# Performance work log

Measured on AMD Instinct MI355X. Metric: run time of the kernel, lower is better.

Reference implementation:

```python
import jax, jax.numpy as jnp
import numpy as np

EPS = 1e-5

def _ln(x, g, b):
    mu = jnp.mean(x, axis=-1, keepdims=True)
    var = jnp.mean((x - mu) ** 2, axis=-1, keepdims=True)
    return (x - mu) / jnp.sqrt(var + EPS) * g + b

def _silu(x):
    return x * jax.nn.sigmoid(x)

def setup_inputs() -> dict:
    key = jax.random.key(0)
    ks = jax.random.split(key, 32)
    B = 131072
    def rn(k, shape, scale=0.05):
        return jax.random.normal(k, shape, dtype=jnp.float32) * scale
    inp = {
        'x': jax.random.normal(ks[0], (B, 90), dtype=jnp.float32),
        'w_emb': rn(ks[1], (24, 10)),
        'pos_d': rn(ks[2], (9, 24), 0.02),
        'pos_c': rn(ks[3], (3, 64), 0.02),
        'tw1': rn(ks[4], (256, 72)), 'tb1': rn(ks[5], (256,)),
        'tw2': rn(ks[6], (256, 256)), 'tb2': rn(ks[7], (256,)),
        'tw3': rn(ks[8], (64, 256)), 'tb3': jnp.zeros((64,), jnp.float32),
        'ln1g': jnp.ones((64,), jnp.float32), 'ln1b': jnp.zeros((64,), jnp.float32),
        'inpw': rn(ks[9], (192, 64)), 'inpb': rn(ks[10], (192,)),
        'outw': rn(ks[11], (64, 64)), 'outb': rn(ks[12], (64,)),
        'ln2g': jnp.ones((64,), jnp.float32), 'ln2b': jnp.zeros((64,), jnp.float32),
        'ffw1': rn(ks[13], (128, 64)), 'ffb1': rn(ks[14], (128,)),
        'ffw2': rn(ks[15], (64, 128)), 'ffb2': rn(ks[16], (64,)),
        'hw1': rn(ks[17], (160, 192)), 'hb1': rn(ks[18], (160,)),
        'hw2': rn(ks[19], (64, 160)), 'hb2': rn(ks[20], (64,)),
        'hw3': rn(ks[21], (1, 64)), 'hb3': jnp.zeros((1,), jnp.float32),
    }
    return inp

def reference(x, w_emb, pos_d, pos_c, tw1, tb1, tw2, tb2, tw3, tb3,
              ln1g, ln1b, inpw, inpb, outw, outb, ln2g, ln2b,
              ffw1, ffb1, ffw2, ffb2, hw1, hb1, hw2, hb2, hw3, hb3):
    B = x.shape[0]
    H, D = 4, 16  # heads, head_dim (embed 64)
    digits = x.reshape(B, 9, 10) @ w_emb.T + pos_d          # [B,9,24]
    chunks = digits.reshape(B, 3, 72)                        # [B,3,72]
    h = _silu(chunks @ tw1.T + tb1)                          # [B,3,256]
    h = _silu(h @ tw2.T + tb2)                               # [B,3,256]
    chunks = h @ tw3.T + tb3                                 # [B,3,64]
    chunks = chunks + pos_c
    a = _ln(chunks, ln1g, ln1b)
    qkv = a @ inpw.T + inpb                                  # [B,3,192]
    q, k, v = jnp.split(qkv, 3, axis=-1)
    q = q.reshape(B, 3, H, D).transpose(0, 2, 1, 3)
    k = k.reshape(B, 3, H, D).transpose(0, 2, 1, 3)
    v = v.reshape(B, 3, H, D).transpose(0, 2, 1, 3)
    scores = jnp.einsum('bhsd,bhtd->bhst', q, k) / jnp.sqrt(jnp.float32(D))
    attn = jax.nn.softmax(scores, axis=-1)
    o = jnp.einsum('bhst,bhtd->bhsd', attn, v)
    o = o.transpose(0, 2, 1, 3).reshape(B, 3, 64)
    attn_out = o @ outw.T + outb
    chunks = chunks + attn_out
    f = _ln(chunks, ln2g, ln2b)
    chunks = chunks + (_silu(f @ ffw1.T + ffb1) @ ffw2.T + ffb2)
    flat = chunks.reshape(B, 192)
    hh = _silu(flat @ hw1.T + hb1)
    hh = _silu(hh @ hw2.T + hb2)
    return hh @ hw3.T + hb3                                  # [B,1]
```

## Files before the change

### kernel.cpp

```cpp
#include <hip/hip_runtime.h>
#include <math.h>


typedef short s8v __attribute__((ext_vector_type(8)));
typedef float f4v __attribute__((ext_vector_type(4)));
typedef int   i2v __attribute__((ext_vector_type(2)));
typedef int   i4v __attribute__((ext_vector_type(4)));

__device__ __forceinline__ short f2bf(float f) {
    unsigned u = __float_as_uint(f);
    unsigned r = (u + 0x7fffu + ((u >> 16) & 1u)) >> 16;
    return (short)r;
}
__device__ __forceinline__ int cvt_pk_bf16(float a, float b) {
    int r;
    asm("v_cvt_pk_bf16_f32 %0, %1, %2" : "=v"(r) : "v"(a), "v"(b));
    return r;
}
__device__ __forceinline__ float silu_f(float v) {
    return v * __builtin_amdgcn_rcpf(1.0f + __expf(-v));
}

#define BARRIER() do {                                        \
    asm volatile("s_waitcnt lgkmcnt(0)" ::: "memory");        \
    __builtin_amdgcn_s_barrier();                             \
    __builtin_amdgcn_sched_barrier(0);                        \
} while (0)

#define OFF_T1F  0
#define OFF_TW2  8192
#define OFF_TW3  73728
#define OFF_INP  90112
#define OFF_OUT  102400
#define OFF_FF1  106496
#define OFF_FF2  114688
#define OFF_HW1  122880
#define OFF_HW2  153600
#define BIAS1_ELEM 163840

__global__ void pack_weights(const float* __restrict__ w_emb, const float* __restrict__ tw1,
                             const float* __restrict__ pos_d, const float* __restrict__ tb1,
                             const float* __restrict__ tw2, const float* __restrict__ tw3,
                             const float* __restrict__ inpw, const float* __restrict__ outw,
                             const float* __restrict__ ffw1, const float* __restrict__ ffw2,
                             const float* __restrict__ hw1, const float* __restrict__ hw2,
                             short* __restrict__ dst)
{
    int L = blockIdx.y;
    if (L == 0) {
        int total = 16 * 512;
        for (int e = blockIdx.x * blockDim.x + threadIdx.x; e < total; e += gridDim.x * blockDim.x) {
            int nt = e >> 9, q = e & 511;
            int l = q >> 3, j = q & 7;
            int n = nt * 16 + (l & 15);
            int k = (l >> 4) * 8 + j;
            float v = 0.f;
            if (k < 30) {
                int gl = k / 10, kk = k - gl * 10;
                const float* trow = tw1 + n * 72 + gl * 24;
                for (int jj = 0; jj < 24; ++jj) v += trow[jj] * w_emb[jj * 10 + kk];
            }
            dst[OFF_T1F + e] = f2bf(v);
        }
        return;
    }
    if (L == 9) {
        float* b1 = (float*)(dst + BIAS1_ELEM);
        for (int e = blockIdx.x * blockDim.x + threadIdx.x; e < 768; e += gridDim.x * blockDim.x) {
            int pos = e >> 8, n = e & 255;
            float v = tb1[n];
            for (int j = 0; j < 72; ++j)
                v += tw1[n * 72 + j] * pos_d[(pos * 3 + j / 24) * 24 + (j % 24)];
            b1[e] = v;
        }
        return;
    }
    const float* W; int K, KS, N, off;
    switch (L) {
      case 1: W = tw2;  K = 256; KS = 8; N = 256; off = OFF_TW2; break;
      case 2: W = tw3;  K = 256; KS = 8; N = 64;  off = OFF_TW3; break;
      case 3: W = inpw; K = 64;  KS = 2; N = 192; off = OFF_INP; break;
      case 4: W = outw; K = 64;  KS = 2; N = 64;  off = OFF_OUT; break;
      case 5: W = ffw1; K = 64;  KS = 2; N = 128; off = OFF_FF1; break;
      case 6: W = ffw2; K = 128; KS = 4; N = 64;  off = OFF_FF2; break;
      case 7: W = hw1;  K = 192; KS = 6; N = 160; off = OFF_HW1; break;
      default:W = hw2;  K = 160; KS = 5; N = 64;  off = OFF_HW2; break;
    }
    int total = (N >> 4) * KS * 512;
    for (int e = blockIdx.x * blockDim.x + threadIdx.x; e < total; e += gridDim.x * blockDim.x) {
        int nt = e / (KS * 512);
        int r  = e - nt * (KS * 512);
        int ks = r >> 9;
        int q  = r & 511;
        int l  = q >> 3, j = q & 7;
        int n  = nt * 16 + (l & 15);
        int k  = ks * 32 + (l >> 4) * 8 + j;
        dst[off + e] = f2bf((k < K) ? W[n * K + k] : 0.0f);
    }
}

template<int KSH> struct PreW { s8v w[KSH]; };

template<int KSH>
__device__ __forceinline__ PreW<KSH> preloadW(const short* __restrict__ Wp,
                                              int lane, int nt, int ksTotal) {
    PreW<KSH> p;
    #pragma unroll
    for (int ks = 0; ks < KSH; ++ks)
        p.w[ks] = *(const s8v*)(Wp + nt * (ksTotal * 512) + ks * 512 + lane * 8);
    return p;
}

template<int EPI, int OP>
__device__ __forceinline__ void epi_store(f4v acc, f4v bv, int t, int n0, void* Out,
                                          const float* __restrict__ aux)
{
    if (EPI == 0 || EPI == 1) {
        float v0 = acc[0] + bv[0], v1 = acc[1] + bv[1];
        float v2 = acc[2] + bv[2], v3 = acc[3] + bv[3];
        if (EPI == 0) { v0 = silu_f(v0); v1 = silu_f(v1); v2 = silu_f(v2); v3 = silu_f(v3); }
        i2v pk; pk[0] = cvt_pk_bf16(v0, v1); pk[1] = cvt_pk_bf16(v2, v3);
        *(i2v*)((short*)Out + t * OP + n0) = pk;
    } else if (EPI == 2) {
        f4v* p = (f4v*)((float*)Out + t * OP + n0);
        f4v o = *p;
        #pragma unroll
        for (int i = 0; i < 4; ++i) o[i] += acc[i] + bv[i];
        *p = o;
    } else if (EPI == 3) {
        f4v pc = *(const f4v*)(aux + (t % 3) * 64 + n0);
        f4v o;
        #pragma unroll
        for (int i = 0; i < 4; ++i) o[i] = acc[i] + bv[i] + pc[i];
        *(f4v*)((float*)Out + t * OP + n0) = o;
    } else if (EPI == 5) {
        f4v ch = *(const f4v*)(aux + t * 68 + n0);
        int rr = t / 3, cc = t - rr * 3;
        i2v pk;
        pk[0] = cvt_pk_bf16(ch[0] + acc[0] + bv[0], ch[1] + acc[1] + bv[1]);
        pk[1] = cvt_pk_bf16(ch[2] + acc[2] + bv[2], ch[3] + acc[3] + bv[3]);
        *(i2v*)((short*)Out + rr * OP + cc * 64 + n0) = pk;
    } else if (EPI == 6) {
        f4v w = *(const f4v*)(aux + n0);
        float p = silu_f(acc[0] + bv[0]) * w[0] + silu_f(acc[1] + bv[1]) * w[1]
                + silu_f(acc[2] + bv[2]) * w[2] + silu_f(acc[3] + bv[3]) * w[3];
        ((float*)Out)[t * OP + (n0 >> 2)] = p;
    } else {
        f4v bp = *(const f4v*)(aux + (t % 3) * 256 + n0);
        float v0 = silu_f(acc[0] + bp[0]), v1 = silu_f(acc[1] + bp[1]);
        float v2 = silu_f(acc[2] + bp[2]), v3 = silu_f(acc[3] + bp[3]);
        i2v pk; pk[0] = cvt_pk_bf16(v0, v1); pk[1] = cvt_pk_bf16(v2, v3);
        *(i2v*)((short*)Out + t * OP + n0) = pk;
    }
}

template<int MT, int KS, int EPI, int AP, int OP>
__device__ __forceinline__ void mfma_T(
    const short* __restrict__ Wp,
    const float* __restrict__ bias,
    const short* A, void* Out, int N,
    const float* __restrict__ aux, int lane, int wid, PreW<KS> pre)
{
    const int l15 = lane & 15, l4 = lane >> 4;
    s8v xf[MT][KS];
    #pragma unroll
    for (int m = 0; m < MT; ++m)
        #pragma unroll
        for (int ks = 0; ks < KS; ++ks)
            xf[m][ks] = *(const s8v*)(A + (m * 16 + l15) * AP + ks * 32 + l4 * 8);

    s8v wf[KS];
    #pragma unroll
    for (int ks = 0; ks < KS; ++ks) wf[ks] = pre.w[ks];

    const int NT = N >> 4;
    for (int nt = wid; nt < NT; nt += 4) {
        s8v wfn[KS];
        const bool more = (nt + 4) < NT;
        if (more) {
            #pragma unroll
            for (int ks = 0; ks < KS; ++ks)
                wfn[ks] = *(const s8v*)(Wp + (nt + 4) * (KS * 512) + ks * 512 + lane * 8);
        }
        const int n0 = nt * 16 + l4 * 4;
        f4v bv = {0.f, 0.f, 0.f, 0.f};
        if (EPI != 7) bv = *(const f4v*)(bias + n0);
        #pragma unroll
        for (int m = 0; m < MT; ++m) {
            f4v acc = {0.f, 0.f, 0.f, 0.f};
            #pragma unroll
            for (int ks = 0; ks < KS; ++ks)
                acc = __builtin_amdgcn_mfma_f32_16x16x32_bf16(wf[ks], xf[m][ks], acc, 0, 0, 0);
            epi_store<EPI, OP>(acc, bv, m * 16 + l15, n0, Out, aux);
        }
        if (more) {
            #pragma unroll
            for (int ks = 0; ks < KS; ++ks) wf[ks] = wfn[ks];
        }
    }
}

template<int OP>
__device__ __forceinline__ void mfma_x1(
    const short* __restrict__ Wp, const float* __restrict__ x, long long row0,
    void* Out, const float* __restrict__ bias1,
    int lane, int wid, PreW<1> pre)
{
    const int l15 = lane & 15, l4 = lane >> 4;
    s8v xf[3];
    #pragma unroll
    for (int m = 0; m < 3; ++m) {
        int t = m * 16 + l15;
        int r = t / 3, c = t - r * 3;
        const float* xp = x + (row0 + r) * 90 + c * 30 + l4 * 8;
        float2 a = *(const float2*)xp;
        float2 b = *(const float2*)(xp + 2);
        float2 d = *(const float2*)(xp + 4);
        float2 e = (l4 < 3) ? *(const float2*)(xp + 6) : make_float2(0.f, 0.f);
        i4v pk;
        pk[0] = cvt_pk_bf16(a.x, a.y);
        pk[1] = cvt_pk_bf16(b.x, b.y);
        pk[2] = cvt_pk_bf16(d.x, d.y);
        pk[3] = cvt_pk_bf16(e.x, e.y);
        xf[m] = *(s8v*)&pk;
    }

    s8v wf = pre.w[0];
    for (int nt = wid; nt < 16; nt += 4) {
        s8v wfn;
        const bool more = (nt + 4) < 16;
        if (more) wfn = *(const s8v*)(Wp + (nt + 4) * 512 + lane * 8);
        const int n0 = nt * 16 + l4 * 4;
        #pragma unroll
        for (int m = 0; m < 3; ++m) {
            f4v acc = {0.f, 0.f, 0.f, 0.f};
            acc = __builtin_amdgcn_mfma_f32_16x16x32_bf16(wf, xf[m], acc, 0, 0, 0);
            epi_store<7, OP>(acc, acc, m * 16 + l15, n0, Out, bias1);
        }
        if (more) wf = wfn;
    }
}

template<int MT, int KSH, int KH, int NTW, int EPI, int AP, int OP>
__device__ __forceinline__ void mfma_acc(
    const short* __restrict__ Wp, const float* __restrict__ bias,
    const short* A, void* Out,
    const float* __restrict__ aux, int lane, int wid, int ntBase, PreW<KSH> pre)
{
    const int l15 = lane & 15, l4 = lane >> 4;
    const int KS = KSH * KH;
    f4v acc[NTW][MT];
    #pragma unroll
    for (int i = 0; i < NTW; ++i)
        #pragma unroll
        for (int m = 0; m < MT; ++m) acc[i][m] = (f4v){0.f, 0.f, 0.f, 0.f};

    s8v wf[KSH];
    #pragma unroll
    for (int ks = 0; ks < KSH; ++ks) wf[ks] = pre.w[ks];

    #pragma unroll
    for (int kh = 0; kh < KH; ++kh) {
        s8v xf[MT][KSH];
        #pragma unroll
        for (int m = 0; m < MT; ++m)
            #pragma unroll
            for (int ks = 0; ks < KSH; ++ks)
                xf[m][ks] = *(const s8v*)(A + (m * 16 + l15) * AP + (kh * KSH + ks) * 32 + l4 * 8);
        #pragma unroll
        for (int i = 0; i < NTW; ++i) {
            s8v wfn[KSH];
            const bool more = (i + 1 < NTW) || (kh + 1 < KH);
            if (more) {
                const int ni  = (i + 1 < NTW) ? i + 1 : 0;
                const int nkh = (i + 1 < NTW) ? kh : kh + 1;
                const int nnt = wid + (ntBase + ni) * 4;
                #pragma unroll
                for (int ks = 0; ks < KSH; ++ks)
                    wfn[ks] = *(const s8v*)(Wp + nnt * (KS * 512) + (nkh * KSH + ks) * 512 + lane * 8);
            }
            #pragma unroll
            for (int m = 0; m < MT; ++m)
                #pragma unroll
                for (int ks = 0; ks < KSH; ++ks)
                    acc[i][m] = __builtin_amdgcn_mfma_f32_16x16x32_bf16(wf[ks], xf[m][ks], acc[i][m], 0, 0, 0);
            if (more) {
                #pragma unroll
                for (int ks = 0; ks < KSH; ++ks) wf[ks] = wfn[ks];
            }
        }
    }
    #pragma unroll
    for (int i = 0; i < NTW; ++i) {
        const int nt = wid + (ntBase + i) * 4;
        const int n0 = nt * 16 + l4 * 4;
        f4v bv = *(const f4v*)(bias + n0);
        #pragma unroll
        for (int m = 0; m < MT; ++m)
            epi_store<EPI, OP>(acc[i][m], bv, m * 16 + l15, n0, Out, aux);
    }
}

__device__ __forceinline__ void ln_phase(const float* CH, short* dst, const int dp,
                                         const float* __restrict__ g,
                                         const float* __restrict__ b, int tid)
{
    if (tid < 192) {
        int t = tid >> 2, p = tid & 3;
        const float* cp = CH + t * 68 + p * 16;
        f4v c[4];
        #pragma unroll
        for (int i = 0; i < 4; ++i) c[i] = *(const f4v*)(cp + i * 4);
        float s = 0.f, ss = 0.f;
        #pragma unroll
        for (int i = 0; i < 4; ++i)
            #pragma unroll
            for (int j = 0; j < 4; ++j) { float v = c[i][j]; s += v; ss += v * v; }
        s += __shfl_xor(s, 1); ss += __shfl_xor(ss, 1);
        s += __shfl_xor(s, 2); ss += __shfl_xor(ss, 2);
        float mu = s * (1.0f / 64.0f);
        float var = ss * (1.0f / 64.0f) - mu * mu;
        float rstd = rsqrtf(var + 1e-5f);
        int pk[8];
        #pragma unroll
        for (int i = 0; i < 4; ++i) {
            f4v gv = *(const f4v*)(g + p * 16 + i * 4);
            f4v bvv = *(const f4v*)(b + p * 16 + i * 4);
            float o0 = (c[i][0] - mu) * rstd * gv[0] + bvv[0];
            float o1 = (c[i][1] - mu) * rstd * gv[1] + bvv[1];
            float o2 = (c[i][2] - mu) * rstd * gv[2] + bvv[2];
            float o3 = (c[i][3] - mu) * rstd * gv[3] + bvv[3];
            pk[i * 2]     = cvt_pk_bf16(o0, o1);
            pk[i * 2 + 1] = cvt_pk_bf16(o2, o3);
        }
        i4v w0 = {pk[0], pk[1], pk[2], pk[3]};
        i4v w1 = {pk[4], pk[5], pk[6], pk[7]};
        *(i4v*)(dst + t * dp + p * 16) = w0;
        *(i4v*)(dst + t * dp + p * 16 + 8) = w1;
    }
}

#define ARENA 25344
#define LDS_BYTES (2 * ARENA)

__global__ __launch_bounds__(256, 3)
void towers_mfma(const float* __restrict__ x,
                 const float* __restrict__ pos_c,
                 const float* __restrict__ tb2, const float* __restrict__ tb3,
                 const float* __restrict__ ln1g, const float* __restrict__ ln1b,
                 const float* __restrict__ inpb, const float* __restrict__ outb,
                 const float* __restrict__ ln2g, const float* __restrict__ ln2b,
                 const float* __restrict__ ffb1, const float* __restrict__ ffb2,
                 const float* __restrict__ hb1, const float* __restrict__ hb2,
                 const float* __restrict__ hw3, const float* __restrict__ hb3,
                 const short* __restrict__ wsBp,
                 float* __restrict__ out)
{
    __shared__ __align__(16) char smem[LDS_BYTES];
    char* P = smem;
    char* Q = smem + ARENA;

    const int tid = threadIdx.x;
    const int lane = tid & 63, wid = tid >> 6;
    const long long row0 = (long long)blockIdx.x * 16;
    const float* bias1 = (const float*)(wsBp + BIAS1_ELEM);

    short* H1 = (short*)P;
    PreW<1> preT1f = preloadW<1>(wsBp + OFF_T1F, lane, wid, 1);
    mfma_x1<264>(wsBp + OFF_T1F, x, row0, H1, bias1, lane, wid, preT1f);
    PreW<4> preT2 = preloadW<4>(wsBp + OFF_TW2, lane, wid, 8);
    BARRIER();

    short* H2 = (short*)Q;
    mfma_acc<3, 4, 2, 2, 0, 264, 264>(wsBp + OFF_TW2, tb2, H1, H2, nullptr, lane, wid, 0, preT2);
    {
        PreW<4> preT2b = preloadW<4>(wsBp + OFF_TW2, lane, wid + 8, 8);
        mfma_acc<3, 4, 2, 2, 0, 264, 264>(wsBp + OFF_TW2, tb2, H1, H2, nullptr, lane, wid, 2, preT2b);
    }
    PreW<4> preT3 = preloadW<4>(wsBp + OFF_TW3, lane, wid, 8);
    BARRIER();

    float* CH = (float*)P;
    mfma_acc<3, 4, 2, 1, 3, 264, 68>(wsBp + OFF_TW3, tb3, H2, CH, pos_c, lane, wid, 0, preT3);
    PreW<2> preINP = preloadW<2>(wsBp + OFF_INP, lane, wid, 2);
    BARRIER();

    short* aln = (short*)(P + 13056);
    ln_phase(CH, aln, 72, ln1g, ln1b, tid);
    BARRIER();

    short* qkv = (short*)Q;
    mfma_T<3, 2, 1, 72, 200>(wsBp + OFF_INP, inpb, aln, qkv, 192, nullptr, lane, wid, preINP);
    PreW<2> preOUT = preloadW<2>(wsBp + OFF_OUT, lane, wid, 2);
    BARRIER();

    short* ao = (short*)(P + 13056);
    if (tid < 192) {
        int r = tid & 15, hc = tid >> 4;
        int h = hc & 3, cq = hc >> 2;
        const short* qp = qkv + (r * 3 + cq) * 200 + h * 16;
        float qv[16];
        { s8v q0 = *(const s8v*)qp, q1 = *(const s8v*)(qp + 8);
          #pragma unroll
          for (int j = 0; j < 8; ++j) {
              qv[j] = __uint_as_float(((unsigned)(unsigned short)q0[j]) << 16);
              qv[8 + j] = __uint_as_float(((unsigned)(unsigned short)q1[j]) << 16);
          } }
        float sc[3];
        #pragma unroll
        for (int c = 0; c < 3; ++c) {
            const short* kp = qkv + (r * 3 + c) * 200 + 64 + h * 16;
            s8v k0 = *(const s8v*)kp, k1 = *(const s8v*)(kp + 8);
            float acc = 0.f;
            #pragma unroll
            for (int j = 0; j < 8; ++j) {
                acc += qv[j] * __uint_as_float(((unsigned)(unsigned short)k0[j]) << 16)
                     + qv[8 + j] * __uint_as_float(((unsigned)(unsigned short)k1[j]) << 16);
            }
            sc[c] = acc * 0.25f;
        }
        float m = fmaxf(sc[0], fmaxf(sc[1], sc[2]));
        float e0 = __expf(sc[0] - m), e1 = __expf(sc[1] - m), e2 = __expf(sc[2] - m);
        float inv = 1.0f / (e0 + e1 + e2);
        e0 *= inv; e1 *= inv; e2 *= inv;
        float ov[16];
        #pragma unroll
        for (int j = 0; j < 16; ++j) ov[j] = 0.f;
        const float ee[3] = {e0, e1, e2};
        #pragma unroll
        for (int c = 0; c < 3; ++c) {
            const short* vp = qkv + (r * 3 + c) * 200 + 128 + h * 16;
            s8v v0 = *(const s8v*)vp, v1 = *(const s8v*)(vp + 8);
            #pragma unroll
            for (int j = 0; j < 8; ++j) {
                ov[j]     += ee[c] * __uint_as_float(((unsigned)(unsigned short)v0[j]) << 16);
                ov[8 + j] += ee[c] * __uint_as_float(((unsigned)(unsigned short)v1[j]) << 16);
            }
        }
        short* op = ao + (r * 3 + cq) * 72 + h * 16;
        i4v pk;
        pk[0] = cvt_pk_bf16(ov[0], ov[1]);   pk[1] = cvt_pk_bf16(ov[2], ov[3]);
        pk[2] = cvt_pk_bf16(ov[4], ov[5]);   pk[3] = cvt_pk_bf16(ov[6], ov[7]);
        *(i4v*)op = pk;
        pk[0] = cvt_pk_bf16(ov[8], ov[9]);   pk[1] = cvt_pk_bf16(ov[10], ov[11]);
        pk[2] = cvt_pk_bf16(ov[12], ov[13]); pk[3] = cvt_pk_bf16(ov[14], ov[15]);
        *(i4v*)(op + 8) = pk;
    }
    BARRIER();

    mfma_T<3, 2, 2, 72, 68>(wsBp + OFF_OUT, outb, ao, CH, 64, nullptr, lane, wid, preOUT);
    PreW<2> preFF1 = preloadW<2>(wsBp + OFF_FF1, lane, wid, 2);
    BARRIER();

    short* fb = (short*)(P + 13056);
    ln_phase(CH, fb, 72, ln2g, ln2b, tid);
    BARRIER();

    short* g1 = (short*)Q;
    mfma_T<3, 2, 0, 72, 136>(wsBp + OFF_FF1, ffb1, fb, g1, 128, nullptr, lane, wid, preFF1);
    PreW<4> preFF2 = preloadW<4>(wsBp + OFF_FF2, lane, wid, 4);
    BARRIER();
    short* flat = (short*)(Q + 13312);
    mfma_T<3, 4, 5, 136, 200>(wsBp + OFF_FF2, ffb2, g1, flat, 64, CH, lane, wid, preFF2);
    PreW<6> preH1 = preloadW<6>(wsBp + OFF_HW1, lane, wid, 6);
    BARRIER();

    short* hh1 = (short*)(P + 13056);
    mfma_T<1, 6, 0, 200, 168>(wsBp + OFF_HW1, hb1, flat, hh1, 160, nullptr, lane, wid, preH1);
    PreW<5> preH2 = preloadW<5>(wsBp + OFF_HW2, lane, wid, 5);
    BARRIER();
    float* part = (float*)Q;
    mfma_T<1, 5, 6, 168, 16>(wsBp + OFF_HW2, hb2, hh1, part, 64, hw3, lane, wid, preH2);
    BARRIER();

    if (tid < 64) {
        int r = tid >> 2, p = tid & 3;
        const float* pp = part + r * 16 + p * 4;
        float acc = pp[0] + pp[1] + pp[2] + pp[3];
        acc += __shfl_xor(acc, 1);
        acc += __shfl_xor(acc, 2);
        if (p == 0) out[row0 + r] = acc + hb3[0];
    }
}

extern "C" void kernel_launch(void* const* d_in, const int* in_sizes, int n_in,
                              void* d_out, int out_size, void* d_ws, size_t ws_size,
                              hipStream_t stream) {
    const float* x     = (const float*)d_in[0];
    const float* w_emb = (const float*)d_in[1];
    const float* pos_d = (const float*)d_in[2];
    const float* pos_c = (const float*)d_in[3];
    const float* tw1   = (const float*)d_in[4];
    const float* tb1   = (const float*)d_in[5];
    const float* tw2   = (const float*)d_in[6];
    const float* tb2   = (const float*)d_in[7];
    const float* tw3   = (const float*)d_in[8];
    const float* tb3   = (const float*)d_in[9];
    const float* ln1g  = (const float*)d_in[10];
    const float* ln1b  = (const float*)d_in[11];
    const float* inpw  = (const float*)d_in[12];
    const float* inpb  = (const float*)d_in[13];
    const float* outw  = (const float*)d_in[14];
    const float* outb  = (const float*)d_in[15];
    const float* ln2g  = (const float*)d_in[16];
    const float* ln2b  = (const float*)d_in[17];
    const float* ffw1  = (const float*)d_in[18];
    const float* ffb1  = (const float*)d_in[19];
    const float* ffw2  = (const float*)d_in[20];
    const float* ffb2  = (const float*)d_in[21];
    const float* hw1   = (const float*)d_in[22];
    const float* hb1   = (const float*)d_in[23];
    const float* hw2   = (const float*)d_in[24];
    const float* hb2   = (const float*)d_in[25];
    const float* hw3   = (const float*)d_in[26];
    const float* hb3   = (const float*)d_in[27];
    float* out = (float*)d_out;
    short* wsBp = (short*)d_ws;

    pack_weights<<<dim3(16, 10), 256, 0, stream>>>(w_emb, tw1, pos_d, tb1,
                                                   tw2, tw3, inpw, outw,
                                                   ffw1, ffw2, hw1, hw2, wsBp);

    const int B = in_sizes[0] / 90;
    towers_mfma<<<B / 16, 256, 0, stream>>>(
        x, pos_c, tb2, tb3,
        ln1g, ln1b, inpb, outb, ln2g, ln2b,
        ffb1, ffb2, hb1, hb2, hw3, hb3, wsBp, out);
}
```

Measured before the change: 228.6 us.

## Compute tower layer 2 in place in LDS to raise occupancy to 4 blocks

Replaces the two-pass tw2 GEMM, which read from one LDS arena and wrote to another, with a single in-place kernel. It holds all 4×3 accumulator tiles in registers, waits on a barrier, then writes the result back over its own input buffer. The LDS buffers are reorganised into one smaller arena (50688 to 39168 bytes) and launch bounds rise from 3 to 4 blocks per CU to improve latency hiding. The cost is more accumulator registers live at once (48 floats), which may cause spills under the tighter register budget, plus an extra barrier.

```diff
diff --git a/kernel.cpp b/kernel.cpp
--- a/kernel.cpp
+++ b/kernel.cpp
@@ -241,6 +241,63 @@
     }
 }
 
+template<int AP>
+__device__ __forceinline__ void mfma_tw2_inplace(
+    const short* __restrict__ Wp, const float* __restrict__ bias,
+    short* H, int lane, int wid, PreW<2> pre)
+{
+    const int l15 = lane & 15, l4 = lane >> 4;
+    f4v acc[4][3];
+    #pragma unroll
+    for (int i = 0; i < 4; ++i)
+        #pragma unroll
+        for (int m = 0; m < 3; ++m) acc[i][m] = (f4v){0.f, 0.f, 0.f, 0.f};
+
+    s8v wf[2];
+    wf[0] = pre.w[0]; wf[1] = pre.w[1];
+
+    #pragma unroll
+    for (int kh = 0; kh < 4; ++kh) {
+        s8v xf[3][2];
+        #pragma unroll
+        for (int m = 0; m < 3; ++m)
+            #pragma unroll
+            for (int ks = 0; ks < 2; ++ks)
+                xf[m][ks] = *(const s8v*)(H + (m * 16 + l15) * AP + (kh * 2 + ks) * 32 + l4 * 8);
+        #pragma unroll
+        for (int i = 0; i < 4; ++i) {
+            s8v wfn[2];
+            const bool more = (i < 3) || (kh < 3);
+            if (more) {
+                const int ni  = (i < 3) ? i + 1 : 0;
+                const int nkh = (i < 3) ? kh : kh + 1;
+                const int nnt = wid + ni * 4;
+                #pragma unroll
+                for (int ks = 0; ks < 2; ++ks)
+                    wfn[ks] = *(const s8v*)(Wp + nnt * (8 * 512) + (nkh * 2 + ks) * 512 + lane * 8);
+            }
+            #pragma unroll
+            for (int m = 0; m < 3; ++m) {
+                acc[i][m] = __builtin_amdgcn_mfma_f32_16x16x32_bf16(wf[0], xf[m][0], acc[i][m], 0, 0, 0);
+                acc[i][m] = __builtin_amdgcn_mfma_f32_16x16x32_bf16(wf[1], xf[m][1], acc[i][m], 0, 0, 0);
+            }
+            if (more) { wf[0] = wfn[0]; wf[1] = wfn[1]; }
+        }
+    }
+
+    BARRIER();
+
+    #pragma unroll
+    for (int i = 0; i < 4; ++i) {
+        const int nt = wid + i * 4;
+        const int n0 = nt * 16 + l4 * 4;
+        f4v bv = *(const f4v*)(bias + n0);
+        #pragma unroll
+        for (int m = 0; m < 3; ++m)
+            epi_store<0, AP>(acc[i][m], bv, m * 16 + l15, n0, H, nullptr);
+    }
+}
+
 template<int MT, int KSH, int KH, int NTW, int EPI, int AP, int OP>
 __device__ __forceinline__ void mfma_acc(
     const short* __restrict__ Wp, const float* __restrict__ bias,
@@ -340,10 +397,9 @@
     }
 }
 
-#define ARENA 25344
-#define LDS_BYTES (2 * ARENA)
-
-__global__ __launch_bounds__(256, 3)
+#define LDS_BYTES 39168
+
+__global__ __launch_bounds__(256, 4)
 void towers_mfma(const float* __restrict__ x,
                  const float* __restrict__ pos_c,
                  const float* __restrict__ tb2, const float* __restrict__ tb3,
@@ -357,44 +413,37 @@
                  float* __restrict__ out)
 {
     __shared__ __align__(16) char smem[LDS_BYTES];
-    char* P = smem;
-    char* Q = smem + ARENA;
 
     const int tid = threadIdx.x;
     const int lane = tid & 63, wid = tid >> 6;
     const long long row0 = (long long)blockIdx.x * 16;
     const float* bias1 = (const float*)(wsBp + BIAS1_ELEM);
 
-    short* H1 = (short*)P;
+    short* H    = (short*)smem;
+    float* CH   = (float*)(smem + 26112);
+    short* tmp7 = (short*)(smem + 19200);
+
     PreW<1> preT1f = preloadW<1>(wsBp + OFF_T1F, lane, wid, 1);
-    mfma_x1<264>(wsBp + OFF_T1F, x, row0, H1, bias1, lane, wid, preT1f);
-    PreW<4> preT2 = preloadW<4>(wsBp + OFF_TW2, lane, wid, 8);
-    BARRIER();
-
-    short* H2 = (short*)Q;
-    mfma_acc<3, 4, 2, 2, 0, 264, 264>(wsBp + OFF_TW2, tb2, H1, H2, nullptr, lane, wid, 0, preT2);
-    {
-        PreW<4> preT2b = preloadW<4>(wsBp + OFF_TW2, lane, wid + 8, 8);
-        mfma_acc<3, 4, 2, 2, 0, 264, 264>(wsBp + OFF_TW2, tb2, H1, H2, nullptr, lane, wid, 2, preT2b);
-    }
+    mfma_x1<264>(wsBp + OFF_T1F, x, row0, H, bias1, lane, wid, preT1f);
+    PreW<2> preT2 = preloadW<2>(wsBp + OFF_TW2, lane, wid, 8);
+    BARRIER();
+
+    mfma_tw2_inplace<264>(wsBp + OFF_TW2, tb2, H, lane, wid, preT2);
     PreW<4> preT3 = preloadW<4>(wsBp + OFF_TW3, lane, wid, 8);
     BARRIER();
 
-    float* CH = (float*)P;
-    mfma_acc<3, 4, 2, 1, 3, 264, 68>(wsBp + OFF_TW3, tb3, H2, CH, pos_c, lane, wid, 0, preT3);
+    mfma_acc<3, 4, 2, 1, 3, 264, 68>(wsBp + OFF_TW3, tb3, H, CH, pos_c, lane, wid, 0, preT3);
     PreW<2> preINP = preloadW<2>(wsBp + OFF_INP, lane, wid, 2);
     BARRIER();
 
-    short* aln = (short*)(P + 13056);
-    ln_phase(CH, aln, 72, ln1g, ln1b, tid);
-    BARRIER();
-
-    short* qkv = (short*)Q;
-    mfma_T<3, 2, 1, 72, 200>(wsBp + OFF_INP, inpb, aln, qkv, 192, nullptr, lane, wid, preINP);
+    ln_phase(CH, tmp7, 72, ln1g, ln1b, tid);
+    BARRIER();
+
+    short* qkv = (short*)smem;
+    mfma_T<3, 2, 1, 72, 200>(wsBp + OFF_INP, inpb, tmp7, qkv, 192, nullptr, lane, wid, preINP);
     PreW<2> preOUT = preloadW<2>(wsBp + OFF_OUT, lane, wid, 2);
     BARRIER();
 
-    short* ao = (short*)(P + 13056);
     if (tid < 192) {
         int r = tid & 15, hc = tid >> 4;
         int h = hc & 3, cq = hc >> 2;
@@ -437,7 +486,7 @@
                 ov[8 + j] += ee[c] * __uint_as_float(((unsigned)(unsigned short)v1[j]) << 16);
             }
         }
-        short* op = ao + (r * 3 + cq) * 72 + h * 16;
+        short* op = tmp7 + (r * 3 + cq) * 72 + h * 16;
         i4v pk;
         pk[0] = cvt_pk_bf16(ov[0], ov[1]);   pk[1] = cvt_pk_bf16(ov[2], ov[3]);
         pk[2] = cvt_pk_bf16(ov[4], ov[5]);   pk[3] = cvt_pk_bf16(ov[6], ov[7]);
@@ -448,28 +497,27 @@
     }
     BARRIER();
 
-    mfma_T<3, 2, 2, 72, 68>(wsBp + OFF_OUT, outb, ao, CH, 64, nullptr, lane, wid, preOUT);
+    mfma_T<3, 2, 2, 72, 68>(wsBp + OFF_OUT, outb, tmp7, CH, 64, nullptr, lane, wid, preOUT);
     PreW<2> preFF1 = preloadW<2>(wsBp + OFF_FF1, lane, wid, 2);
     BARRIER();
 
-    short* fb = (short*)(P + 13056);
-    ln_phase(CH, fb, 72, ln2g, ln2b, tid);
-    BARRIER();
-
-    short* g1 = (short*)Q;
-    mfma_T<3, 2, 0, 72, 136>(wsBp + OFF_FF1, ffb1, fb, g1, 128, nullptr, lane, wid, preFF1);
+    ln_phase(CH, tmp7, 72, ln2g, ln2b, tid);
+    BARRIER();
+
+    short* g1 = (short*)smem;
+    mfma_T<3, 2, 0, 72, 136>(wsBp + OFF_FF1, ffb1, tmp7, g1, 128, nullptr, lane, wid, preFF1);
     PreW<4> preFF2 = preloadW<4>(wsBp + OFF_FF2, lane, wid, 4);
     BARRIER();
-    short* flat = (short*)(Q + 13312);
+    short* flat = (short*)(smem + 13056);
     mfma_T<3, 4, 5, 136, 200>(wsBp + OFF_FF2, ffb2, g1, flat, 64, CH, lane, wid, preFF2);
     PreW<6> preH1 = preloadW<6>(wsBp + OFF_HW1, lane, wid, 6);
     BARRIER();
 
-    short* hh1 = (short*)(P + 13056);
+    short* hh1 = (short*)smem;
     mfma_T<1, 6, 0, 200, 168>(wsBp + OFF_HW1, hb1, flat, hh1, 160, nullptr, lane, wid, preH1);
     PreW<5> preH2 = preloadW<5>(wsBp + OFF_HW2, lane, wid, 5);
     BARRIER();
-    float* part = (float*)Q;
+    float* part = (float*)(smem + 8192);
     mfma_T<1, 5, 6, 168, 16>(wsBp + OFF_HW2, hb2, hh1, part, 64, hw3, lane, wid, preH2);
     BARRIER();
 
```

Result: faster. 209.4 us (-8.4%).
